# Performance work log

Measured on AMD Instinct MI355X. Metric: run time of the kernel, lower is better.

Reference implementation:

```python
import jax, jax.numpy as jnp
import numpy as np

VOCAB, HIDDEN, EMB_DIM = 30522, 768, 128
B, QLEN, DLEN = 1024, 32, 180
NEG = -1e4  # masked doc-token similarity
EPS = 1e-12


def setup_inputs() -> dict:
    key = jax.random.key(0)
    k1, k2, k3, k4, k5, k6 = jax.random.split(key, 6)
    return {
        "query_input_ids": jax.random.randint(k1, (B, QLEN), 0, VOCAB, dtype=jnp.int64) if jax.config.jax_enable_x64 else jax.random.randint(k1, (B, QLEN), 0, VOCAB, dtype=jnp.int32),
        "query_attention_mask": jax.random.randint(k2, (B, QLEN), 0, 2, dtype=jnp.int32),
        "doc_input_ids": jax.random.randint(k3, (B, DLEN), 0, VOCAB, dtype=jnp.int32),
        "doc_attention_mask": jax.random.randint(k4, (B, DLEN), 0, 2, dtype=jnp.int32),
        "embed_table": jax.random.normal(k5, (VOCAB, HIDDEN), dtype=jnp.float32) * 0.02,
        "proj_w": jax.random.normal(k6, (HIDDEN, EMB_DIM), dtype=jnp.float32) * 0.02,
        "proj_b": jnp.zeros((EMB_DIM,), dtype=jnp.float32),
    }


def _encode(ids, embed_table, proj_w, proj_b):
    # token embedding lookup -> linear projection -> L2 normalize (ColBERT-style)
    h = embed_table[ids]                      # (B, L, HIDDEN)
    e = jnp.einsum('blh,hd->bld', h, proj_w) + proj_b  # (B, L, EMB_DIM)
    e = e / (jnp.linalg.norm(e, axis=-1, keepdims=True) + EPS)
    return e


def reference(query_input_ids, query_attention_mask, doc_input_ids,
              doc_attention_mask, embed_table, proj_w, proj_b):
    q = _encode(query_input_ids, embed_table, proj_w, proj_b)  # (B, Q, D)
    d = _encode(doc_input_ids, embed_table, proj_w, proj_b)    # (B, T, D)
    # Batched MaxSim: sim[b,q,t] = <q_emb, d_emb>
    sim = jnp.einsum('bqd,btd->bqt', q, d)
    sim = jnp.where(doc_attention_mask[:, None, :] > 0, sim, NEG)
    max_sim = sim.max(axis=-1)                                  # (B, Q)
    scores = (max_sim * query_attention_mask.astype(max_sim.dtype)).sum(axis=-1)
    return scores  # (B,)
```

## Files before the change

kernel.cpp:

```cpp
#include <hip/hip_runtime.h>
#include <math.h>

#define VOCAB  30522
#define HIDDEN 768
#define EMB    128
#define BATCH  1024
#define QLEN   32
#define DLEN   180
#define NEGV   (-1e4f)

typedef __attribute__((ext_vector_type(8))) short bf16x8;
typedef __attribute__((ext_vector_type(4))) float f32x4;

__device__ __forceinline__ unsigned short f2bf(float x) {
  union { float f; unsigned u; } v; v.f = x;
  unsigned r = v.u + 0x7FFFu + ((v.u >> 16) & 1u);
  return (unsigned short)(r >> 16);
}
__device__ __forceinline__ float bf2f(unsigned short h) {
  union { float f; unsigned u; } v; v.u = ((unsigned)h) << 16;
  return v.f;
}
__device__ __forceinline__ void split_pk(float x0, float x1, unsigned& h, unsigned& l) {
  asm("v_cvt_pk_bf16_f32 %0, %1, %2" : "=v"(h) : "v"(x0), "v"(x1));
  float h0, h1;
  h0 = __uint_as_float(h << 16);
  h1 = __uint_as_float(h & 0xffff0000u);
  float l0 = x0 - h0, l1 = x1 - h1;
  asm("v_cvt_pk_bf16_f32 %0, %1, %2" : "=v"(l) : "v"(l0), "v"(l1));
}

__global__ __launch_bounds__(256) void prep_wfrag(
    const float* __restrict__ W, unsigned short* __restrict__ wfh,
    unsigned short* __restrict__ wfl) {
  int g = blockIdx.x * 256 + threadIdx.x;
  if (g >= 24 * 8 * 64) return;
  int lane = g & 63, nt = (g >> 6) & 7, kk = g >> 9;
  int lr = lane & 15, kq = lane >> 4;
  int n = nt * 16 + lr;
  int k0 = kk * 32 + kq * 8;
  unsigned short hh[8], ll[8];
#pragma unroll
  for (int j = 0; j < 8; ++j) {
    float x = W[(size_t)(k0 + j) * EMB + n];
    unsigned short hi = f2bf(x);
    hh[j] = hi;
    ll[j] = f2bf(x - bf2f(hi));
  }
  size_t base = (size_t)g * 8;
#pragma unroll
  for (int j = 0; j < 2; ++j) {
    *(ushort4*)(wfh + base + j * 4) = *(ushort4*)(hh + j * 4);
    *(ushort4*)(wfl + base + j * 4) = *(ushort4*)(ll + j * 4);
  }
}

__global__ __launch_bounds__(256) void colbert_proj_mfma(
    const float* __restrict__ emb, const unsigned short* __restrict__ wfh,
    const unsigned short* __restrict__ wfl, const float* __restrict__ bias,
    unsigned short* __restrict__ pebf) {
  __shared__ __align__(16) char smem[34816];

  const int tid  = threadIdx.x;
  const int lane = tid & 63;
  const int wid  = tid >> 6;
  const int wm   = wid & 1;
  const int wn   = wid >> 1;
  const int lr   = lane & 15;
  const int kq   = lane >> 4;
  const int row0 = blockIdx.x * 64;

  const int srow = tid >> 4;
  const int sc4  = tid & 15;

  f32x4 acc[2][4];
#pragma unroll
  for (int mi = 0; mi < 2; ++mi)
#pragma unroll
    for (int ni = 0; ni < 4; ++ni) acc[mi][ni] = (f32x4)0.f;

  float4 ar[4];
#pragma unroll
  for (int i = 0; i < 4; ++i) {
    int row = i * 16 + srow;
    int gr = row0 + row; if (gr > VOCAB - 1) gr = VOCAB - 1;
    ar[i] = *(const float4*)(emb + (size_t)gr * HIDDEN + sc4 * 4);
  }

#define WRITE_A(bufidx)                                                        \
  {                                                                            \
    char* Ahb = smem + (bufidx) * 16384;                                       \
    char* Alb = Ahb + 8192;                                                    \
    _Pragma("unroll")                                                          \
    for (int i = 0; i < 4; ++i) {                                              \
      int row = i * 16 + srow;                                                 \
      unsigned h0, l0, h1, l1;                                                 \
      split_pk(ar[i].x, ar[i].y, h0, l0);                                      \
      split_pk(ar[i].z, ar[i].w, h1, l1);                                      \
      int byt = (row * 128 + sc4 * 8) ^ ((row & 7) << 4);                      \
      *(uint2*)(Ahb + byt) = make_uint2(h0, h1);                               \
      *(uint2*)(Alb + byt) = make_uint2(l0, l1);                               \
    }                                                                          \
  }

  WRITE_A(0);
  __syncthreads();

  for (int hc = 0; hc < 12; ++hc) {
    const int cur = hc & 1;
    if (hc < 11) {
#pragma unroll
      for (int i = 0; i < 4; ++i) {
        int row = i * 16 + srow;
        int gr = row0 + row; if (gr > VOCAB - 1) gr = VOCAB - 1;
        ar[i] = *(const float4*)(emb + (size_t)gr * HIDDEN + (hc + 1) * 64 + sc4 * 4);
      }
    }
    char* Ahb = smem + cur * 16384;
    char* Alb = Ahb + 8192;
#pragma unroll
    for (int kk = 0; kk < 2; ++kk) {
      bf16x8 bh[4], bl[4];
      size_t bbase = ((size_t)((hc * 2 + kk) * 8 + wn * 4) * 64 + lane) * 8;
#pragma unroll
      for (int ni = 0; ni < 4; ++ni) {
        bh[ni] = *(const bf16x8*)(wfh + bbase + ni * 512);
        bl[ni] = *(const bf16x8*)(wfl + bbase + ni * 512);
      }
      bf16x8 ah[2], al[2];
#pragma unroll
      for (int mi = 0; mi < 2; ++mi) {
        int row = wm * 32 + mi * 16 + lr;
        int byt = (row * 128 + kk * 64 + kq * 16) ^ ((row & 7) << 4);
        ah[mi] = *(bf16x8*)(Ahb + byt);
        al[mi] = *(bf16x8*)(Alb + byt);
      }
#pragma unroll
      for (int mi = 0; mi < 2; ++mi)
#pragma unroll
        for (int ni = 0; ni < 4; ++ni) {
          acc[mi][ni] = __builtin_amdgcn_mfma_f32_16x16x32_bf16(ah[mi], bh[ni], acc[mi][ni], 0, 0, 0);
          acc[mi][ni] = __builtin_amdgcn_mfma_f32_16x16x32_bf16(ah[mi], bl[ni], acc[mi][ni], 0, 0, 0);
          acc[mi][ni] = __builtin_amdgcn_mfma_f32_16x16x32_bf16(al[mi], bh[ni], acc[mi][ni], 0, 0, 0);
        }
    }
    if (hc < 11) WRITE_A(cur ^ 1);
    __syncthreads();
  }

  float* ep = (float*)smem;
#pragma unroll
  for (int ni = 0; ni < 4; ++ni) {
    int col = wn * 64 + ni * 16 + lr;
    float bb = bias[col];
#pragma unroll
    for (int mi = 0; mi < 2; ++mi)
#pragma unroll
      for (int j = 0; j < 4; ++j) {
        int r = wm * 32 + mi * 16 + kq * 4 + j;
        ep[r * 132 + col] = acc[mi][ni][j] + bb;
      }
  }
  __syncthreads();
  {
    int row = tid >> 2, quad = tid & 3;
    float4 vv[8];
    float ss = 0.f;
#pragma unroll
    for (int i = 0; i < 8; ++i) {
      vv[i] = *(float4*)&ep[row * 132 + quad * 32 + i * 4];
      ss += vv[i].x * vv[i].x + vv[i].y * vv[i].y + vv[i].z * vv[i].z + vv[i].w * vv[i].w;
    }
    ss += __shfl_xor(ss, 1);
    ss += __shfl_xor(ss, 2);
    float sc = 1.f / (sqrtf(ss) + 1e-12f);
    int gr = row0 + row;
    if (gr < VOCAB) {
#pragma unroll
      for (int i = 0; i < 8; ++i) {
        ushort4 o;
        o.x = f2bf(vv[i].x * sc); o.y = f2bf(vv[i].y * sc);
        o.z = f2bf(vv[i].z * sc); o.w = f2bf(vv[i].w * sc);
        *(ushort4*)&pebf[(size_t)gr * EMB + quad * 32 + i * 4] = o;
      }
    }
  }
}

__global__ __launch_bounds__(256) void colbert_score_mfma(
    const int* __restrict__ qids, const int* __restrict__ qmask,
    const int* __restrict__ dids, const int* __restrict__ dmask,
    const unsigned short* __restrict__ pebf, float* __restrict__ out) {
  __shared__ int sqid[32];
  __shared__ int sdid[192];
  __shared__ unsigned char smsk[192];
  __shared__ float wmax[4][32];

  const int b    = blockIdx.x;
  const int tid  = threadIdx.x;
  const int lane = tid & 63;
  const int wid  = tid >> 6;
  const int lr   = lane & 15;
  const int kq   = lane >> 4;

  if (tid < 32) sqid[tid] = qids[b * QLEN + tid];
  if (tid < 192) {
    if (tid < DLEN) {
      sdid[tid] = dids[b * DLEN + tid];
      smsk[tid] = (unsigned char)(dmask[b * DLEN + tid] > 0 ? 1 : 0);
    } else {
      sdid[tid] = 0;
      smsk[tid] = 0;
    }
  }
  __syncthreads();

  bf16x8 af[2][4];
#pragma unroll
  for (int mi = 0; mi < 2; ++mi) {
    size_t base = (size_t)sqid[mi * 16 + lr] * EMB + kq * 8;
#pragma unroll
    for (int ks = 0; ks < 4; ++ks)
      af[mi][ks] = *(const bf16x8*)(pebf + base + ks * 32);
  }
  const int n0 = wid * 48;
  bf16x8 bf[3][4];
#pragma unroll
  for (int ni = 0; ni < 3; ++ni) {
    size_t base = (size_t)sdid[n0 + ni * 16 + lr] * EMB + kq * 8;
#pragma unroll
    for (int ks = 0; ks < 4; ++ks)
      bf[ni][ks] = *(const bf16x8*)(pebf + base + ks * 32);
  }

  f32x4 acc[2][3];
#pragma unroll
  for (int mi = 0; mi < 2; ++mi)
#pragma unroll
    for (int ni = 0; ni < 3; ++ni) acc[mi][ni] = (f32x4)0.f;

#pragma unroll
  for (int ks = 0; ks < 4; ++ks)
#pragma unroll
    for (int mi = 0; mi < 2; ++mi)
#pragma unroll
      for (int ni = 0; ni < 3; ++ni)
        acc[mi][ni] = __builtin_amdgcn_mfma_f32_16x16x32_bf16(af[mi][ks], bf[ni][ks], acc[mi][ni], 0, 0, 0);

#pragma unroll
  for (int mi = 0; mi < 2; ++mi) {
#pragma unroll
    for (int j = 0; j < 4; ++j) {
      float m = -3.0e38f;
#pragma unroll
      for (int ni = 0; ni < 3; ++ni) {
        int t = n0 + ni * 16 + lr;
        float s = smsk[t] ? acc[mi][ni][j] : NEGV;
        m = fmaxf(m, s);
      }
#pragma unroll
      for (int x = 1; x < 16; x <<= 1) m = fmaxf(m, __shfl_xor(m, x));
      if (lr == 0) wmax[wid][mi * 16 + kq * 4 + j] = m;
    }
  }
  __syncthreads();

  if (tid < 32) {
    float m = fmaxf(fmaxf(wmax[0][tid], wmax[1][tid]),
                    fmaxf(wmax[2][tid], wmax[3][tid]));
    float s = m * (float)qmask[b * QLEN + tid];
#pragma unroll
    for (int x = 1; x < 32; x <<= 1) s += __shfl_xor(s, x);
    if (tid == 0) out[b] = s;
  }
}

extern "C" void kernel_launch(void* const* d_in, const int* in_sizes, int n_in,
                              void* d_out, int out_size, void* d_ws, size_t ws_size,
                              hipStream_t stream) {
  const int*   qids  = (const int*)d_in[0];
  const int*   qmask = (const int*)d_in[1];
  const int*   dids  = (const int*)d_in[2];
  const int*   dmask = (const int*)d_in[3];
  const float* emb   = (const float*)d_in[4];
  const float* W     = (const float*)d_in[5];
  const float* bias  = (const float*)d_in[6];
  float*       out   = (float*)d_out;

  char* ws = (char*)d_ws;
  unsigned short* pebf = (unsigned short*)ws;
  unsigned short* wfh  = (unsigned short*)(ws + 7813632);
  unsigned short* wfl  = (unsigned short*)(ws + 7813632 + 196608);

  prep_wfrag<<<48, 256, 0, stream>>>(W, wfh, wfl);
  colbert_proj_mfma<<<(VOCAB + 63) / 64, 256, 0, stream>>>(emb, wfh, wfl, bias, pebf);
  colbert_score_mfma<<<BATCH, 256, 0, stream>>>(qids, qmask, dids, dmask, pebf, out);
}
```

Before: 48.96 us.

## Retile vocab projection to 32-row blocks with 128-wide K chunks

The projection kernel now gives each block 32 vocab rows instead of 64, which doubles the grid to about 954 blocks. Each of the 4 waves owns a 32-column slice across all rows. The K loop uses 128-wide chunks over 6 iterations, so there are half as many barriers, and all weight fragments for a chunk are loaded before the next embedding prefetch, separated by a sched_barrier. The epilogue uses 8 threads per row and writes 16-byte stores. The larger grid spreads work across more CUs, but each block reuses its weight-fragment loads over fewer rows.

```diff
diff --git a/kernel.cpp b/kernel.cpp
--- a/kernel.cpp
+++ b/kernel.cpp
@@ -59,32 +59,28 @@
     const float* __restrict__ emb, const unsigned short* __restrict__ wfh,
     const unsigned short* __restrict__ wfl, const float* __restrict__ bias,
     unsigned short* __restrict__ pebf) {
-  __shared__ __align__(16) char smem[34816];
+  __shared__ __align__(16) char smem[32768];
 
   const int tid  = threadIdx.x;
   const int lane = tid & 63;
   const int wid  = tid >> 6;
-  const int wm   = wid & 1;
-  const int wn   = wid >> 1;
   const int lr   = lane & 15;
   const int kq   = lane >> 4;
-  const int row0 = blockIdx.x * 64;
-
-  const int srow = tid >> 4;
-  const int sc4  = tid & 15;
-
-  f32x4 acc[2][4];
+  const int row0 = blockIdx.x * 32;
+
+  f32x4 acc[2][2];
 #pragma unroll
   for (int mi = 0; mi < 2; ++mi)
 #pragma unroll
-    for (int ni = 0; ni < 4; ++ni) acc[mi][ni] = (f32x4)0.f;
+    for (int ni = 0; ni < 2; ++ni) acc[mi][ni] = (f32x4)0.f;
 
   float4 ar[4];
 #pragma unroll
   for (int i = 0; i < 4; ++i) {
-    int row = i * 16 + srow;
+    int idx = i * 256 + tid;
+    int row = idx >> 5, c4 = idx & 31;
     int gr = row0 + row; if (gr > VOCAB - 1) gr = VOCAB - 1;
-    ar[i] = *(const float4*)(emb + (size_t)gr * HIDDEN + sc4 * 4);
+    ar[i] = *(const float4*)(emb + (size_t)gr * HIDDEN + c4 * 4);
   }
 
 #define WRITE_A(bufidx)                                                        \
@@ -93,11 +89,12 @@
     char* Alb = Ahb + 8192;                                                    \
     _Pragma("unroll")                                                          \
     for (int i = 0; i < 4; ++i) {                                              \
-      int row = i * 16 + srow;                                                 \
+      int idx = i * 256 + tid;                                                 \
+      int row = idx >> 5, c4 = idx & 31;                                       \
       unsigned h0, l0, h1, l1;                                                 \
       split_pk(ar[i].x, ar[i].y, h0, l0);                                      \
       split_pk(ar[i].z, ar[i].w, h1, l1);                                      \
-      int byt = (row * 128 + sc4 * 8) ^ ((row & 7) << 4);                      \
+      int byt = (row * 256 + c4 * 8) ^ ((row & 7) << 4);                       \
       *(uint2*)(Ahb + byt) = make_uint2(h0, h1);                               \
       *(uint2*)(Alb + byt) = make_uint2(l0, l1);                               \
     }                                                                          \
@@ -106,83 +103,90 @@
   WRITE_A(0);
   __syncthreads();
 
-  for (int hc = 0; hc < 12; ++hc) {
+  for (int hc = 0; hc < 6; ++hc) {
     const int cur = hc & 1;
-    if (hc < 11) {
+    bf16x8 bh[4][2], bl[4][2];
+#pragma unroll
+    for (int kk = 0; kk < 4; ++kk)
+#pragma unroll
+      for (int ni = 0; ni < 2; ++ni) {
+        size_t g = ((size_t)((hc * 4 + kk) * 8 + wid * 2 + ni) * 64 + lane) * 8;
+        bh[kk][ni] = *(const bf16x8*)(wfh + g);
+        bl[kk][ni] = *(const bf16x8*)(wfl + g);
+      }
+    __builtin_amdgcn_sched_barrier(0);
+    if (hc < 5) {
 #pragma unroll
       for (int i = 0; i < 4; ++i) {
-        int row = i * 16 + srow;
+        int idx = i * 256 + tid;
+        int row = idx >> 5, c4 = idx & 31;
         int gr = row0 + row; if (gr > VOCAB - 1) gr = VOCAB - 1;
-        ar[i] = *(const float4*)(emb + (size_t)gr * HIDDEN + (hc + 1) * 64 + sc4 * 4);
+        ar[i] = *(const float4*)(emb + (size_t)gr * HIDDEN + (hc + 1) * 128 + c4 * 4);
       }
     }
     char* Ahb = smem + cur * 16384;
     char* Alb = Ahb + 8192;
 #pragma unroll
-    for (int kk = 0; kk < 2; ++kk) {
-      bf16x8 bh[4], bl[4];
-      size_t bbase = ((size_t)((hc * 2 + kk) * 8 + wn * 4) * 64 + lane) * 8;
-#pragma unroll
-      for (int ni = 0; ni < 4; ++ni) {
-        bh[ni] = *(const bf16x8*)(wfh + bbase + ni * 512);
-        bl[ni] = *(const bf16x8*)(wfl + bbase + ni * 512);
-      }
+    for (int kk = 0; kk < 4; ++kk) {
       bf16x8 ah[2], al[2];
 #pragma unroll
       for (int mi = 0; mi < 2; ++mi) {
-        int row = wm * 32 + mi * 16 + lr;
-        int byt = (row * 128 + kk * 64 + kq * 16) ^ ((row & 7) << 4);
+        int row = mi * 16 + lr;
+        int byt = (row * 256 + kk * 64 + kq * 16) ^ ((row & 7) << 4);
         ah[mi] = *(bf16x8*)(Ahb + byt);
         al[mi] = *(bf16x8*)(Alb + byt);
       }
 #pragma unroll
       for (int mi = 0; mi < 2; ++mi)
 #pragma unroll
-        for (int ni = 0; ni < 4; ++ni) {
-          acc[mi][ni] = __builtin_amdgcn_mfma_f32_16x16x32_bf16(ah[mi], bh[ni], acc[mi][ni], 0, 0, 0);
-          acc[mi][ni] = __builtin_amdgcn_mfma_f32_16x16x32_bf16(ah[mi], bl[ni], acc[mi][ni], 0, 0, 0);
-          acc[mi][ni] = __builtin_amdgcn_mfma_f32_16x16x32_bf16(al[mi], bh[ni], acc[mi][ni], 0, 0, 0);
+        for (int ni = 0; ni < 2; ++ni) {
+          acc[mi][ni] = __builtin_amdgcn_mfma_f32_16x16x32_bf16(ah[mi], bh[kk][ni], acc[mi][ni], 0, 0, 0);
+          acc[mi][ni] = __builtin_amdgcn_mfma_f32_16x16x32_bf16(ah[mi], bl[kk][ni], acc[mi][ni], 0, 0, 0);
+          acc[mi][ni] = __builtin_amdgcn_mfma_f32_16x16x32_bf16(al[mi], bh[kk][ni], acc[mi][ni], 0, 0, 0);
         }
     }
-    if (hc < 11) WRITE_A(cur ^ 1);
+    if (hc < 5) WRITE_A(cur ^ 1);
     __syncthreads();
   }
 
   float* ep = (float*)smem;
 #pragma unroll
-  for (int ni = 0; ni < 4; ++ni) {
-    int col = wn * 64 + ni * 16 + lr;
+  for (int ni = 0; ni < 2; ++ni) {
+    int col = wid * 32 + ni * 16 + lr;
     float bb = bias[col];
 #pragma unroll
     for (int mi = 0; mi < 2; ++mi)
 #pragma unroll
       for (int j = 0; j < 4; ++j) {
-        int r = wm * 32 + mi * 16 + kq * 4 + j;
+        int r = mi * 16 + kq * 4 + j;
         ep[r * 132 + col] = acc[mi][ni][j] + bb;
       }
   }
   __syncthreads();
   {
-    int row = tid >> 2, quad = tid & 3;
-    float4 vv[8];
+    int row = tid >> 3, oct = tid & 7;
+    float4 vv[4];
     float ss = 0.f;
 #pragma unroll
-    for (int i = 0; i < 8; ++i) {
-      vv[i] = *(float4*)&ep[row * 132 + quad * 32 + i * 4];
+    for (int i = 0; i < 4; ++i) {
+      vv[i] = *(float4*)&ep[row * 132 + oct * 16 + i * 4];
       ss += vv[i].x * vv[i].x + vv[i].y * vv[i].y + vv[i].z * vv[i].z + vv[i].w * vv[i].w;
     }
     ss += __shfl_xor(ss, 1);
     ss += __shfl_xor(ss, 2);
+    ss += __shfl_xor(ss, 4);
     float sc = 1.f / (sqrtf(ss) + 1e-12f);
     int gr = row0 + row;
     if (gr < VOCAB) {
-#pragma unroll
-      for (int i = 0; i < 8; ++i) {
-        ushort4 o;
-        o.x = f2bf(vv[i].x * sc); o.y = f2bf(vv[i].y * sc);
-        o.z = f2bf(vv[i].z * sc); o.w = f2bf(vv[i].w * sc);
-        *(ushort4*)&pebf[(size_t)gr * EMB + quad * 32 + i * 4] = o;
-      }
+      unsigned pk[8];
+#pragma unroll
+      for (int i = 0; i < 4; ++i) {
+        pk[i * 2 + 0] = (unsigned)f2bf(vv[i].x * sc) | ((unsigned)f2bf(vv[i].y * sc) << 16);
+        pk[i * 2 + 1] = (unsigned)f2bf(vv[i].z * sc) | ((unsigned)f2bf(vv[i].w * sc) << 16);
+      }
+      uint4* dst = (uint4*)(pebf + (size_t)gr * EMB + oct * 16);
+      dst[0] = make_uint4(pk[0], pk[1], pk[2], pk[3]);
+      dst[1] = make_uint4(pk[4], pk[5], pk[6], pk[7]);
     }
   }
 }
@@ -224,13 +228,13 @@
       af[mi][ks] = *(const bf16x8*)(pebf + base + ks * 32);
   }
   const int n0 = wid * 48;
-  bf16x8 bf[3][4];
+  bf16x8 bfr[3][4];
 #pragma unroll
   for (int ni = 0; ni < 3; ++ni) {
     size_t base = (size_t)sdid[n0 + ni * 16 + lr] * EMB + kq * 8;
 #pragma unroll
     for (int ks = 0; ks < 4; ++ks)
-      bf[ni][ks] = *(const bf16x8*)(pebf + base + ks * 32);
+      bfr[ni][ks] = *(const bf16x8*)(pebf + base + ks * 32);
   }
 
   f32x4 acc[2][3];
@@ -245,7 +249,7 @@
     for (int mi = 0; mi < 2; ++mi)
 #pragma unroll
       for (int ni = 0; ni < 3; ++ni)
-        acc[mi][ni] = __builtin_amdgcn_mfma_f32_16x16x32_bf16(af[mi][ks], bf[ni][ks], acc[mi][ni], 0, 0, 0);
+        acc[mi][ni] = __builtin_amdgcn_mfma_f32_16x16x32_bf16(af[mi][ks], bfr[ni][ks], acc[mi][ni], 0, 0, 0);
 
 #pragma unroll
   for (int mi = 0; mi < 2; ++mi) {
@@ -293,6 +297,6 @@
   unsigned short* wfl  = (unsigned short*)(ws + 7813632 + 196608);
 
   prep_wfrag<<<48, 256, 0, stream>>>(W, wfh, wfl);
-  colbert_proj_mfma<<<(VOCAB + 63) / 64, 256, 0, stream>>>(emb, wfh, wfl, bias, pebf);
+  colbert_proj_mfma<<<(VOCAB + 31) / 32, 256, 0, stream>>>(emb, wfh, wfl, bias, pebf);
   colbert_score_mfma<<<BATCH, 256, 0, stream>>>(qids, qmask, dids, dmask, pebf, out);
 }
```

Measured after the change: 49.75 us. No clear change (+1.6%).

## Restructure vocab projection: A fragments in registers, weight fragments double-buffered in LDS

Applied to the files above, without the earlier changes.

The projection kernel moves to 32-row tiles and 128-thread blocks. Each wave now loads its embedding rows straight from global memory into MFMA-layout registers and splits them into bf16 hi/lo there, so the A operand no longer passes through LDS. The preformatted weight fragments are staged through a double-buffered LDS tile that both waves share, replacing the per-wave global reads of weights. Output stores are widened to 16-byte vectors. The trade-off is more blocks, each doing less reuse per tile, plus tighter register pressure from the prefetch registers.

```diff
diff --git a/kernel.cpp b/kernel.cpp
--- a/kernel.cpp
+++ b/kernel.cpp
@@ -55,111 +55,98 @@
   }
 }
 
-__global__ __launch_bounds__(256) void colbert_proj_mfma(
+__global__ __launch_bounds__(128) void colbert_proj_mfma(
     const float* __restrict__ emb, const unsigned short* __restrict__ wfh,
     const unsigned short* __restrict__ wfl, const float* __restrict__ bias,
     unsigned short* __restrict__ pebf) {
-  __shared__ __align__(16) char smem[34816];
+  __shared__ __align__(16) char smem[32768];
 
   const int tid  = threadIdx.x;
   const int lane = tid & 63;
-  const int wid  = tid >> 6;
-  const int wm   = wid & 1;
-  const int wn   = wid >> 1;
+  const int wm   = tid >> 6;
   const int lr   = lane & 15;
   const int kq   = lane >> 4;
-  const int row0 = blockIdx.x * 64;
-
-  const int srow = tid >> 4;
-  const int sc4  = tid & 15;
-
-  f32x4 acc[2][4];
-#pragma unroll
-  for (int mi = 0; mi < 2; ++mi)
-#pragma unroll
-    for (int ni = 0; ni < 4; ++ni) acc[mi][ni] = (f32x4)0.f;
-
-  float4 ar[4];
-#pragma unroll
-  for (int i = 0; i < 4; ++i) {
-    int row = i * 16 + srow;
-    int gr = row0 + row; if (gr > VOCAB - 1) gr = VOCAB - 1;
-    ar[i] = *(const float4*)(emb + (size_t)gr * HIDDEN + sc4 * 4);
-  }
-
-#define WRITE_A(bufidx)                                                        \
+  const int row0 = blockIdx.x * 32;
+
+  int grow = row0 + wm * 16 + lr;
+  if (grow > VOCAB - 1) grow = VOCAB - 1;
+  const float* aptr = emb + (size_t)grow * HIDDEN + kq * 8;
+
+  f32x4 acc[8];
+#pragma unroll
+  for (int nt = 0; nt < 8; ++nt) acc[nt] = (f32x4)0.f;
+
+  float4 arA[2][2];
+  uint4  breg[8];
+
+#define BLOAD(T)                                                               \
   {                                                                            \
-    char* Ahb = smem + (bufidx) * 16384;                                       \
-    char* Alb = Ahb + 8192;                                                    \
     _Pragma("unroll")                                                          \
     for (int i = 0; i < 4; ++i) {                                              \
-      int row = i * 16 + srow;                                                 \
-      unsigned h0, l0, h1, l1;                                                 \
-      split_pk(ar[i].x, ar[i].y, h0, l0);                                      \
-      split_pk(ar[i].z, ar[i].w, h1, l1);                                      \
-      int byt = (row * 128 + sc4 * 8) ^ ((row & 7) << 4);                      \
-      *(uint2*)(Ahb + byt) = make_uint2(h0, h1);                               \
-      *(uint2*)(Alb + byt) = make_uint2(l0, l1);                               \
-    }                                                                          \
-  }
-
-  WRITE_A(0);
-  __syncthreads();
-
-  for (int hc = 0; hc < 12; ++hc) {
-    const int cur = hc & 1;
-    if (hc < 11) {
-#pragma unroll
-      for (int i = 0; i < 4; ++i) {
-        int row = i * 16 + srow;
-        int gr = row0 + row; if (gr > VOCAB - 1) gr = VOCAB - 1;
-        ar[i] = *(const float4*)(emb + (size_t)gr * HIDDEN + (hc + 1) * 64 + sc4 * 4);
-      }
-    }
-    char* Ahb = smem + cur * 16384;
-    char* Alb = Ahb + 8192;
-#pragma unroll
-    for (int kk = 0; kk < 2; ++kk) {
-      bf16x8 bh[4], bl[4];
-      size_t bbase = ((size_t)((hc * 2 + kk) * 8 + wn * 4) * 64 + lane) * 8;
-#pragma unroll
-      for (int ni = 0; ni < 4; ++ni) {
-        bh[ni] = *(const bf16x8*)(wfh + bbase + ni * 512);
-        bl[ni] = *(const bf16x8*)(wfl + bbase + ni * 512);
-      }
-      bf16x8 ah[2], al[2];
-#pragma unroll
-      for (int mi = 0; mi < 2; ++mi) {
-        int row = wm * 32 + mi * 16 + lr;
-        int byt = (row * 128 + kk * 64 + kq * 16) ^ ((row & 7) << 4);
-        ah[mi] = *(bf16x8*)(Ahb + byt);
-        al[mi] = *(bf16x8*)(Alb + byt);
-      }
-#pragma unroll
-      for (int mi = 0; mi < 2; ++mi)
-#pragma unroll
-        for (int ni = 0; ni < 4; ++ni) {
-          acc[mi][ni] = __builtin_amdgcn_mfma_f32_16x16x32_bf16(ah[mi], bh[ni], acc[mi][ni], 0, 0, 0);
-          acc[mi][ni] = __builtin_amdgcn_mfma_f32_16x16x32_bf16(ah[mi], bl[ni], acc[mi][ni], 0, 0, 0);
-          acc[mi][ni] = __builtin_amdgcn_mfma_f32_16x16x32_bf16(al[mi], bh[ni], acc[mi][ni], 0, 0, 0);
-        }
-    }
-    if (hc < 11) WRITE_A(cur ^ 1);
-    __syncthreads();
+      size_t s = (size_t)(T) * 4096 + (size_t)(i * 128 + tid) * 8;             \
+      breg[i]     = *(const uint4*)(wfh + s);                                  \
+      breg[4 + i] = *(const uint4*)(wfl + s);                                  \
+    }                                                                          \
+  }
+
+#define BWRITE(BUF)                                                            \
+  {                                                                            \
+    char* d = smem + (BUF) * 16384;                                            \
+    _Pragma("unroll")                                                          \
+    for (int i = 0; i < 4; ++i) {                                              \
+      *(uint4*)(d + (i * 128 + tid) * 16)        = breg[i];                    \
+      *(uint4*)(d + 8192 + (i * 128 + tid) * 16) = breg[4 + i];                \
+    }                                                                          \
+  }
+
+  BLOAD(0);
+  arA[0][0] = *(const float4*)(aptr);
+  arA[0][1] = *(const float4*)(aptr + 4);
+  arA[1][0] = *(const float4*)(aptr + 32);
+  arA[1][1] = *(const float4*)(aptr + 36);
+  BWRITE(0);
+  BLOAD(1);
+  __syncthreads();
+
+#define CHUNK(T, P)                                                            \
+  {                                                                            \
+    union { unsigned u[4]; bf16x8 v; } Ah_, Al_;                               \
+    split_pk(arA[P][0].x, arA[P][0].y, Ah_.u[0], Al_.u[0]);                    \
+    split_pk(arA[P][0].z, arA[P][0].w, Ah_.u[1], Al_.u[1]);                    \
+    split_pk(arA[P][1].x, arA[P][1].y, Ah_.u[2], Al_.u[2]);                    \
+    split_pk(arA[P][1].z, arA[P][1].w, Ah_.u[3], Al_.u[3]);                    \
+    if ((T) + 1 < 24) BWRITE((P) ^ 1);           \
+    if ((T) + 2 < 24) {                                                        \
+      BLOAD((T) + 2);                          \
+      arA[P][0] = *(const float4*)(aptr + ((T) + 2) * 32);                     \
+      arA[P][1] = *(const float4*)(aptr + ((T) + 2) * 32 + 4);                 \
+    }                                                                          \
+    char* rb = smem + (P) * 16384;                                             \
+    _Pragma("unroll")                                                          \
+    for (int nt = 0; nt < 8; ++nt) {                                           \
+      bf16x8 bh = *(bf16x8*)(rb + nt * 1024 + lane * 16);                      \
+      bf16x8 bl = *(bf16x8*)(rb + 8192 + nt * 1024 + lane * 16);               \
+      acc[nt] = __builtin_amdgcn_mfma_f32_16x16x32_bf16(Ah_.v, bh, acc[nt], 0, 0, 0); \
+      acc[nt] = __builtin_amdgcn_mfma_f32_16x16x32_bf16(Ah_.v, bl, acc[nt], 0, 0, 0); \
+      acc[nt] = __builtin_amdgcn_mfma_f32_16x16x32_bf16(Al_.v, bh, acc[nt], 0, 0, 0); \
+    }                                                                          \
+    __syncthreads();                                                           \
+  }
+
+  for (int tt = 0; tt < 24; tt += 2) {
+    CHUNK(tt, 0);
+    CHUNK(tt + 1, 1);
   }
 
   float* ep = (float*)smem;
 #pragma unroll
-  for (int ni = 0; ni < 4; ++ni) {
-    int col = wn * 64 + ni * 16 + lr;
-    float bb = bias[col];
-#pragma unroll
-    for (int mi = 0; mi < 2; ++mi)
-#pragma unroll
-      for (int j = 0; j < 4; ++j) {
-        int r = wm * 32 + mi * 16 + kq * 4 + j;
-        ep[r * 132 + col] = acc[mi][ni][j] + bb;
-      }
+  for (int nt = 0; nt < 8; ++nt) {
+    float bb = bias[nt * 16 + lr];
+#pragma unroll
+    for (int j = 0; j < 4; ++j) {
+      int r = wm * 16 + kq * 4 + j;
+      ep[r * 132 + nt * 16 + lr] = acc[nt][j] + bb;
+    }
   }
   __syncthreads();
   {
@@ -176,15 +163,22 @@
     float sc = 1.f / (sqrtf(ss) + 1e-12f);
     int gr = row0 + row;
     if (gr < VOCAB) {
+      unsigned pk[16];
 #pragma unroll
       for (int i = 0; i < 8; ++i) {
-        ushort4 o;
-        o.x = f2bf(vv[i].x * sc); o.y = f2bf(vv[i].y * sc);
-        o.z = f2bf(vv[i].z * sc); o.w = f2bf(vv[i].w * sc);
-        *(ushort4*)&pebf[(size_t)gr * EMB + quad * 32 + i * 4] = o;
+        pk[i * 2 + 0] = (unsigned)f2bf(vv[i].x * sc) | ((unsigned)f2bf(vv[i].y * sc) << 16);
+        pk[i * 2 + 1] = (unsigned)f2bf(vv[i].z * sc) | ((unsigned)f2bf(vv[i].w * sc) << 16);
       }
-    }
-  }
+      uint4* dst = (uint4*)(pebf + (size_t)gr * EMB + quad * 32);
+      dst[0] = make_uint4(pk[0],  pk[1],  pk[2],  pk[3]);
+      dst[1] = make_uint4(pk[4],  pk[5],  pk[6],  pk[7]);
+      dst[2] = make_uint4(pk[8],  pk[9],  pk[10], pk[11]);
+      dst[3] = make_uint4(pk[12], pk[13], pk[14], pk[15]);
+    }
+  }
+#undef BLOAD
+#undef BWRITE
+#undef CHUNK
 }
 
 __global__ __launch_bounds__(256) void colbert_score_mfma(
@@ -224,13 +218,13 @@
       af[mi][ks] = *(const bf16x8*)(pebf + base + ks * 32);
   }
   const int n0 = wid * 48;
-  bf16x8 bf[3][4];
+  bf16x8 bfr[3][4];
 #pragma unroll
   for (int ni = 0; ni < 3; ++ni) {
     size_t base = (size_t)sdid[n0 + ni * 16 + lr] * EMB + kq * 8;
 #pragma unroll
     for (int ks = 0; ks < 4; ++ks)
-      bf[ni][ks] = *(const bf16x8*)(pebf + base + ks * 32);
+      bfr[ni][ks] = *(const bf16x8*)(pebf + base + ks * 32);
   }
 
   f32x4 acc[2][3];
@@ -245,7 +239,7 @@
     for (int mi = 0; mi < 2; ++mi)
 #pragma unroll
       for (int ni = 0; ni < 3; ++ni)
-        acc[mi][ni] = __builtin_amdgcn_mfma_f32_16x16x32_bf16(af[mi][ks], bf[ni][ks], acc[mi][ni], 0, 0, 0);
+        acc[mi][ni] = __builtin_amdgcn_mfma_f32_16x16x32_bf16(af[mi][ks], bfr[ni][ks], acc[mi][ni], 0, 0, 0);
 
 #pragma unroll
   for (int mi = 0; mi < 2; ++mi) {
@@ -293,6 +287,6 @@
   unsigned short* wfl  = (unsigned short*)(ws + 7813632 + 196608);
 
   prep_wfrag<<<48, 256, 0, stream>>>(W, wfh, wfl);
-  colbert_proj_mfma<<<(VOCAB + 63) / 64, 256, 0, stream>>>(emb, wfh, wfl, bias, pebf);
+  colbert_proj_mfma<<<(VOCAB + 31) / 32, 128, 0, stream>>>(emb, wfh, wfl, bias, pebf);
   colbert_score_mfma<<<BATCH, 256, 0, stream>>>(qids, qmask, dids, dmask, pebf, out);
 }
```

After: 130.0 us. 2.65x slower.
